# Optimization experiments

Hardware: AMD Instinct MI355X
Metric: run time of the kernel (lower is better)

Reference implementation:

```python
import jax, jax.numpy as jnp
import numpy as np

B, S, HID, NH = 4, 1024, 1024, 16
DK = HID // NH
SCALE = DK ** -0.5
NEG = -9e15


def setup_inputs() -> dict:
    key = jax.random.key(0)
    ks = jax.random.split(key, 10)
    std = HID ** -0.5
    return {
        "batch": jax.random.normal(ks[0], (B, S, HID), jnp.float32),
        "attn_bias": jax.random.normal(ks[1], (B, NH, S, S), jnp.float32),
        "Wq": jax.random.normal(ks[2], (HID, HID), jnp.float32) * std,
        "bq": jnp.zeros((HID,), jnp.float32),
        "Wk": jax.random.normal(ks[3], (HID, HID), jnp.float32) * std,
        "bk": jnp.zeros((HID,), jnp.float32),
        "Wv": jax.random.normal(ks[4], (HID, HID), jnp.float32) * std,
        "bv": jnp.zeros((HID,), jnp.float32),
        "Wo": jax.random.normal(ks[5], (HID, HID), jnp.float32) * std,
        "bo": jnp.zeros((HID,), jnp.float32),
    }


def reference(batch, attn_bias, Wq, bq, Wk, bk, Wv, bv, Wo, bo):
    b, s, _ = batch.shape
    # QKV projections -> [b, h, s, d]
    q = (batch @ Wq.T + bq).reshape(b, s, NH, DK).transpose(0, 2, 1, 3)
    k = (batch @ Wk.T + bk).reshape(b, s, NH, DK).transpose(0, 2, 1, 3)
    v = (batch @ Wv.T + bv).reshape(b, s, NH, DK).transpose(0, 2, 1, 3)
    # scaled scores [b, h, s, s]
    x = jnp.einsum("bhqd,bhkd->bhqk", q * SCALE, k)
    # custom zero-mask: exact zeros become -9e15
    x = jnp.where(x == 0, jnp.float32(NEG), x)
    x = x + attn_bias
    p = jax.nn.softmax(x, axis=3)  # dropout_rate=0.0 -> identity
    o = jnp.einsum("bhqk,bhkd->bhqd", p, v)
    o = o.transpose(0, 2, 1, 3).reshape(b, s, NH * DK)
    return o @ Wo.T + bo
```

## Files before the change

### kernel.cpp

```cpp
#include <hip/hip_runtime.h>
#include <hip/hip_bf16.h>
#include <stdint.h>
#include <stddef.h>

#define Bd  4
#define Sd  1024
#define Hd  1024
#define NHd 16
#define DKd 64
#define SCALEF 0.125f
#define NEGV  -9.0e15f
#define L2E   1.4426950408889634f

typedef __attribute__((ext_vector_type(8))) short bfrag;
typedef __attribute__((ext_vector_type(4))) float facc;
typedef __attribute__((ext_vector_type(4))) float f32x4;

typedef __attribute__((address_space(1))) const unsigned int ga_u32;
typedef __attribute__((address_space(3))) unsigned int ls_u32;

__device__ __forceinline__ void gload_lds16(const void* g, void* l) {
  __builtin_amdgcn_global_load_lds((ga_u32*)g, (ls_u32*)l, 16, 0, 0);
}

__device__ __forceinline__ unsigned short f2bf(float f) {
  unsigned int u = __float_as_uint(f);
  u += 0x7fffu + ((u >> 16) & 1u);
  return (unsigned short)(u >> 16);
}

__global__ void castk_all(const float* __restrict__ s0, const float* __restrict__ s1,
                          const float* __restrict__ s2, const float* __restrict__ s3,
                          const float* __restrict__ s4,
                          unsigned short* __restrict__ d0, unsigned short* __restrict__ d1,
                          unsigned short* __restrict__ d2, unsigned short* __restrict__ d3,
                          unsigned short* __restrict__ d4) {
  const int id = blockIdx.x;
  const float* s; unsigned short* d; int i;
  if (id < 4096) { s = s0; d = d0; i = id * 256 + threadIdx.x; }
  else {
    const int w = (id - 4096) >> 10;
    s = (w == 0) ? s1 : (w == 1) ? s2 : (w == 2) ? s3 : s4;
    d = (w == 0) ? d1 : (w == 1) ? d2 : (w == 2) ? d3 : d4;
    i = ((id - 4096) & 1023) * 256 + threadIdx.x;
  }
  float4 v = ((const float4*)s)[i];
  ushort4 ov;
  ov.x = f2bf(v.x); ov.y = f2bf(v.y); ov.z = f2bf(v.z); ov.w = f2bf(v.w);
  ((ushort4*)d)[i] = ov;
}

__global__ __launch_bounds__(256, 3)
void gemm_qkv(const unsigned short* __restrict__ A,
              const unsigned short* __restrict__ W0, const unsigned short* __restrict__ W1,
              const unsigned short* __restrict__ W2,
              const float* __restrict__ b0, const float* __restrict__ b1, const float* __restrict__ b2,
              unsigned short* __restrict__ o0, unsigned short* __restrict__ o1, unsigned short* __restrict__ o2) {
  __shared__ __align__(16) unsigned short smem[128 * 136];
  const int z = blockIdx.z;
  const unsigned short* Bm = (z == 0) ? W0 : (z == 1) ? W1 : W2;
  const float* bias = (z == 0) ? b0 : (z == 1) ? b1 : b2;
  unsigned short* out = (z == 0) ? o0 : (z == 1) ? o1 : o2;

  const int m0 = blockIdx.x * 128, n0 = blockIdx.y * 128;
  const int tid = threadIdx.x;
  const int wave = tid >> 6, lane = tid & 63;
  const int quad = lane >> 4, l16 = lane & 15;
  const int wm = wave >> 1, wn = wave & 1;

  facc acc[4][4] = {};

  const int j0 = wave * 128 + lane;
  const int j1 = j0 + 64;
  const int row0 = j0 >> 2, ko0 = (j0 & 3) << 3;
  const int row1 = j1 >> 2, ko1 = (j1 & 3) << 3;
  const size_t aoff0 = (size_t)(m0 + row0) * 1024 + ko0;
  const size_t aoff1 = (size_t)(m0 + row1) * 1024 + ko1;
  const size_t boff0 = (size_t)(n0 + row0) * 1024 + ko0;
  const size_t boff1 = (size_t)(n0 + row1) * 1024 + ko1;

  const int stA = (wave * 2 + 0) * 512;
  const int stA1i = (wave * 2 + 1) * 512;

  gload_lds16(A + aoff0, smem + stA);
  gload_lds16(A + aoff1, smem + stA1i);
  gload_lds16(Bm + boff0, smem + 8192 + stA);
  gload_lds16(Bm + boff1, smem + 8192 + stA1i);
  __syncthreads();

  for (int k0 = 0; k0 < 1024; k0 += 32) {
    const int cur = (k0 >> 5) & 1;
    const int nxt = cur ^ 1;
    if (k0 < 992) {
      unsigned short* dA = smem + nxt * 4096;
      unsigned short* dB = smem + 8192 + nxt * 4096;
      gload_lds16(A + aoff0 + k0 + 32, dA + stA);
      gload_lds16(A + aoff1 + k0 + 32, dA + stA1i);
      gload_lds16(Bm + boff0 + k0 + 32, dB + stA);
      gload_lds16(Bm + boff1 + k0 + 32, dB + stA1i);
    }
    const unsigned short* sA = smem + cur * 4096;
    const unsigned short* sB = smem + 8192 + cur * 4096;
    bfrag af[4], bf[4];
#pragma unroll
    for (int i = 0; i < 4; ++i) af[i] = *(const bfrag*)(sA + (wm * 64 + i * 16 + l16) * 32 + quad * 8);
#pragma unroll
    for (int j = 0; j < 4; ++j) bf[j] = *(const bfrag*)(sB + (wn * 64 + j * 16 + l16) * 32 + quad * 8);
#pragma unroll
    for (int i = 0; i < 4; ++i)
#pragma unroll
      for (int j = 0; j < 4; ++j)
        acc[i][j] = __builtin_amdgcn_mfma_f32_16x16x32_bf16(af[i], bf[j], acc[i][j], 0, 0, 0);
    __syncthreads();
  }

  if (z < 2) {
#pragma unroll
    for (int i = 0; i < 4; ++i)
#pragma unroll
      for (int j = 0; j < 4; ++j) {
        const int col = n0 + wn * 64 + j * 16 + l16;
        const float bv = bias[col];
        const int h = col >> 6, d = col & 63;
#pragma unroll
        for (int r = 0; r < 4; ++r) {
          const int m = m0 + wm * 64 + i * 16 + quad * 4 + r;
          const int b = m >> 10, s = m & 1023;
          out[(((size_t)(b * NHd + h) * Sd) + s) * DKd + d] = f2bf(acc[i][j][r] + bv);
        }
      }
  } else {
    unsigned short* sT = smem;
#pragma unroll
    for (int i = 0; i < 4; ++i)
#pragma unroll
      for (int j = 0; j < 4; ++j) {
        const int col = n0 + wn * 64 + j * 16 + l16;
        const float bv = bias[col];
        const int nrow = wn * 64 + j * 16 + l16;
        const int mbase = wm * 64 + i * 16 + quad * 4;
        ushort4 pk;
        pk.x = f2bf(acc[i][j][0] + bv);
        pk.y = f2bf(acc[i][j][1] + bv);
        pk.z = f2bf(acc[i][j][2] + bv);
        pk.w = f2bf(acc[i][j][3] + bv);
        *(ushort4*)(sT + nrow * 136 + mbase) = pk;
      }
    __syncthreads();
    const int bI = m0 >> 10, s0i = m0 & 1023;
#pragma unroll
    for (int it = 0; it < 8; ++it) {
      const int c = tid + it * 256;
      const int row = c >> 4, mc = (c & 15) * 8;
      bfrag vv = *(const bfrag*)(sT + row * 136 + mc);
      const int col = n0 + row, hh = col >> 6, dd = col & 63;
      *(bfrag*)(out + (((size_t)(bI * NHd + hh) * DKd) + dd) * Sd + s0i + mc) = vv;
    }
  }
}

__global__ __launch_bounds__(256, 3)
void gemm_out(const unsigned short* __restrict__ A, const unsigned short* __restrict__ Bm,
              const float* __restrict__ bias, float* __restrict__ out) {
  __shared__ __align__(16) unsigned short smem[24576];
  const int m0 = blockIdx.x * 64, n0 = blockIdx.y * 128;
  const int tid = threadIdx.x;
  const int wave = tid >> 6, lane = tid & 63;
  const int quad = lane >> 4, l16 = lane & 15;

  facc acc[8] = {};

  const int cA0 = (wave * 2 + 0) * 64 + lane;
  const int cA1 = (wave * 2 + 1) * 64 + lane;
  const int rA0 = cA0 >> 3, kA0 = ((cA0 & 7) ^ (rA0 & 7)) * 8;
  const int rA1 = cA1 >> 3, kA1 = ((cA1 & 7) ^ (rA1 & 7)) * 8;
  const size_t aoff0 = (size_t)(m0 + rA0) * 1024 + kA0;
  const size_t aoff1 = (size_t)(m0 + rA1) * 1024 + kA1;
  size_t boff[4];
#pragma unroll
  for (int i = 0; i < 4; ++i) {
    const int c = (wave * 4 + i) * 64 + lane;
    const int r = c >> 3, kk = ((c & 7) ^ (r & 7)) * 8;
    boff[i] = (size_t)(n0 + r) * 1024 + kk;
  }

  const int stA0 = (wave * 2 + 0) * 512;
  const int stA1i = (wave * 2 + 1) * 512;

  gload_lds16(A + aoff0, smem + stA0);
  gload_lds16(A + aoff1, smem + stA1i);
#pragma unroll
  for (int i = 0; i < 4; ++i)
    gload_lds16(Bm + boff[i], smem + 8192 + (wave * 4 + i) * 512);
  __syncthreads();

  for (int k0 = 0; k0 < 1024; k0 += 64) {
    const int cur = (k0 >> 6) & 1;
    const int nxt = cur ^ 1;
    if (k0 < 960) {
      unsigned short* dA = smem + nxt * 4096;
      unsigned short* dB = smem + 8192 + nxt * 8192;
      gload_lds16(A + aoff0 + k0 + 64, dA + stA0);
      gload_lds16(A + aoff1 + k0 + 64, dA + stA1i);
#pragma unroll
      for (int i = 0; i < 4; ++i)
        gload_lds16(Bm + boff[i] + k0 + 64, dB + (wave * 4 + i) * 512);
    }
    const unsigned short* sA = smem + cur * 4096;
    const unsigned short* sB = smem + 8192 + cur * 8192;
#pragma unroll
    for (int c2 = 0; c2 < 2; ++c2) {
      const int ko = ((c2 * 4 + quad) ^ (l16 & 7)) * 8;
      bfrag af = *(const bfrag*)(sA + (wave * 16 + l16) * 64 + ko);
#pragma unroll
      for (int j = 0; j < 8; ++j) {
        bfrag bf = *(const bfrag*)(sB + (j * 16 + l16) * 64 + ko);
        acc[j] = __builtin_amdgcn_mfma_f32_16x16x32_bf16(af, bf, acc[j], 0, 0, 0);
      }
    }
    __syncthreads();
  }

#pragma unroll
  for (int j = 0; j < 8; ++j) {
    const int col = n0 + j * 16 + l16;
    const float bv = bias[col];
#pragma unroll
    for (int r = 0; r < 4; ++r) {
      const int m = m0 + wave * 16 + quad * 4 + r;
      out[(size_t)m * 1024 + col] = acc[j][r] + bv;
    }
  }
}

__global__ __attribute__((amdgpu_flat_work_group_size(512, 512), amdgpu_waves_per_eu(4, 4)))
void attn_kernel(const unsigned short* __restrict__ q,
                 const unsigned short* __restrict__ k,
                 const unsigned short* __restrict__ vt,
                 const float* __restrict__ bias,
                 unsigned short* __restrict__ o)
{
  __shared__ __align__(16) unsigned short sK[2][64 * 64];
  __shared__ __align__(16) unsigned short sV[2][64 * 64];
  __shared__ __align__(16) unsigned int sP[8][16][36];

  const int p = blockIdx.x;
  const int xcd = p & 7;
  const int g = p >> 3;
  const int bh = ((g >> 3) << 3) | xcd;
  const int qblk = g & 7;
  const int tid = threadIdx.x;
  const int wave = tid >> 6, lane = tid & 63;
  const int quad = lane >> 4, l16 = lane & 15;
  const int b = bh >> 4, h = bh & 15;

  const unsigned short* qh = q + (size_t)bh * Sd * DKd;
  const unsigned short* kh = k + (size_t)bh * Sd * DKd;
  const unsigned short* vh = vt + (size_t)bh * DKd * Sd;
  const float* bias_h = bias + (size_t)bh * Sd * Sd;
  const int rq = qblk * 128 + wave * 16;
  unsigned int (*sPw)[36] = sP[wave];

  const int srow = wave * 8 + (lane >> 3);
  const int sslot = (lane & 7) ^ (srow & 7);
  const unsigned short* srcK = kh + (size_t)srow * DKd + sslot * 8;
  const unsigned short* srcV = vh + (size_t)srow * Sd + sslot * 8;
  unsigned short* dK0 = sK[0] + wave * 512;
  unsigned short* dK1 = sK[1] + wave * 512;
  unsigned short* dV0 = sV[0] + wave * 512;
  unsigned short* dV1 = sV[1] + wave * 512;

  const int xs0 = ((0 + quad) ^ (l16 & 7)) * 8;
  const int xs1 = ((4 + quad) ^ (l16 & 7)) * 8;

  bfrag qf[2];
#pragma unroll
  for (int c = 0; c < 2; ++c)
    qf[c] = *(const bfrag*)(qh + (size_t)(rq + l16) * DKd + c * 32 + quad * 8);

  facc oacc[4] = {};
  float lsum = 0.f;
  const float SL2 = SCALEF * L2E;

  const float* bpS = bias_h + (size_t)(rq + l16) * Sd + quad * 4;
  f32x4 br0 = __builtin_nontemporal_load((const f32x4*)(bpS + 0));
  f32x4 br1 = __builtin_nontemporal_load((const f32x4*)(bpS + 16));
  f32x4 br2 = __builtin_nontemporal_load((const f32x4*)(bpS + 32));
  f32x4 br3 = __builtin_nontemporal_load((const f32x4*)(bpS + 48));

  gload_lds16(srcK, dK0);
  gload_lds16(srcV, dV0);
  __syncthreads();

  for (int t = 0; t < 16; ++t) {
    const int bb = t & 1;
    if (t < 15) {
      const int kn = (t + 1) * 64;
      gload_lds16(srcK + (size_t)kn * DKd, bb ? dK0 : dK1);
      gload_lds16(srcV + kn, bb ? dV0 : dV1);
    }
    const unsigned short* sKb = sK[bb];
    const unsigned short* sVb = sV[bb];
    facc sacc[4] = {};
#pragma unroll
    for (int j = 0; j < 4; ++j) {
      bfrag kf = *(const bfrag*)(sKb + (j * 16 + l16) * 64 + xs0);
      sacc[j] = __builtin_amdgcn_mfma_f32_16x16x32_bf16(kf, qf[0], sacc[j], 0, 0, 0);
    }
#pragma unroll
    for (int j = 0; j < 4; ++j) {
      bfrag kf = *(const bfrag*)(sKb + (j * 16 + l16) * 64 + xs1);
      sacc[j] = __builtin_amdgcn_mfma_f32_16x16x32_bf16(kf, qf[1], sacc[j], 0, 0, 0);
    }
    asm volatile("" : "+v"(br0), "+v"(br1), "+v"(br2), "+v"(br3));
    unsigned int pk[4][2];
#pragma unroll
    for (int j = 0; j < 4; ++j) {
      const f32x4 bv = (j == 0) ? br0 : (j == 1) ? br1 : (j == 2) ? br2 : br3;
      float e0 = __builtin_amdgcn_exp2f(fmaf(sacc[j][0], SL2, bv.x * L2E));
      float e1 = __builtin_amdgcn_exp2f(fmaf(sacc[j][1], SL2, bv.y * L2E));
      float e2 = __builtin_amdgcn_exp2f(fmaf(sacc[j][2], SL2, bv.z * L2E));
      float e3 = __builtin_amdgcn_exp2f(fmaf(sacc[j][3], SL2, bv.w * L2E));
      e0 = (sacc[j][0] == 0.f) ? 0.f : e0;
      e1 = (sacc[j][1] == 0.f) ? 0.f : e1;
      e2 = (sacc[j][2] == 0.f) ? 0.f : e2;
      e3 = (sacc[j][3] == 0.f) ? 0.f : e3;
      lsum += (e0 + e1) + (e2 + e3);
      pk[j][0] = (unsigned int)f2bf(e0) | ((unsigned int)f2bf(e1) << 16);
      pk[j][1] = (unsigned int)f2bf(e2) | ((unsigned int)f2bf(e3) << 16);
    }
    if (t < 15) {
      const float* bpn = bpS + (t + 1) * 64;
      br0 = __builtin_nontemporal_load((const f32x4*)(bpn + 0));
      br1 = __builtin_nontemporal_load((const f32x4*)(bpn + 16));
      br2 = __builtin_nontemporal_load((const f32x4*)(bpn + 32));
      br3 = __builtin_nontemporal_load((const f32x4*)(bpn + 48));
    }
#pragma unroll
    for (int j = 0; j < 4; ++j) {
      uint2 w; w.x = pk[j][0]; w.y = pk[j][1];
      *(uint2*)&sPw[l16][j * 8 + quad * 2] = w;
    }
#pragma unroll
    for (int c = 0; c < 2; ++c) {
      bfrag pf = *(const bfrag*)&sPw[l16][c * 16 + quad * 4];
      const int xsc = c ? xs1 : xs0;
#pragma unroll
      for (int n = 0; n < 4; ++n) {
        bfrag vf = *(const bfrag*)(sVb + (n * 16 + l16) * 64 + xsc);
        oacc[n] = __builtin_amdgcn_mfma_f32_16x16x32_bf16(vf, pf, oacc[n], 0, 0, 0);
      }
    }
    __syncthreads();
  }

  lsum += __shfl_xor(lsum, 16, 64);
  lsum += __shfl_xor(lsum, 32, 64);
  const float rinv = 1.0f / lsum;

  const size_t rowo = (size_t)(b * Sd + rq + l16) * Hd + h * 64 + quad * 4;
#pragma unroll
  for (int n = 0; n < 4; ++n) {
    ushort4 st;
    st.x = f2bf(oacc[n][0] * rinv);
    st.y = f2bf(oacc[n][1] * rinv);
    st.z = f2bf(oacc[n][2] * rinv);
    st.w = f2bf(oacc[n][3] * rinv);
    *(ushort4*)(o + rowo + n * 16) = st;
  }
}

extern "C" void kernel_launch(void* const* d_in, const int* in_sizes, int n_in,
                              void* d_out, int out_size, void* d_ws, size_t ws_size,
                              hipStream_t stream) {
  const float* batch = (const float*)d_in[0];
  const float* attn_bias = (const float*)d_in[1];
  const float* Wq = (const float*)d_in[2];
  const float* bq = (const float*)d_in[3];
  const float* Wk = (const float*)d_in[4];
  const float* bk = (const float*)d_in[5];
  const float* Wv = (const float*)d_in[6];
  const float* bv = (const float*)d_in[7];
  const float* Wo = (const float*)d_in[8];
  const float* bo = (const float*)d_in[9];
  float* out = (float*)d_out;

  unsigned short* ws = (unsigned short*)d_ws;
  unsigned short* Ab  = ws;
  unsigned short* Wqb = Ab  + 4194304;
  unsigned short* Wkb = Wqb + 1048576;
  unsigned short* Wvb = Wkb + 1048576;
  unsigned short* Wob = Wvb + 1048576;
  unsigned short* qb  = Wob + 1048576;
  unsigned short* kb  = qb  + 4194304;
  unsigned short* vtb = kb  + 4194304;
  unsigned short* ob  = vtb + 4194304;

  castk_all<<<8192, 256, 0, stream>>>(batch, Wq, Wk, Wv, Wo, Ab, Wqb, Wkb, Wvb, Wob);
  gemm_qkv<<<dim3(32, 8, 3), 256, 0, stream>>>(Ab, Wqb, Wkb, Wvb, bq, bk, bv, qb, kb, vtb);
  attn_kernel<<<dim3(512), 512, 0, stream>>>(qb, kb, vtb, attn_bias, ob);
  gemm_out<<<dim3(64, 8), 256, 0, stream>>>(ob, Wob, bo, out);
}
```

Before: 450.2 us.

## Stage attention bias through LDS via async loads and halve KV tile size

The attention kernel now streams the fp32 bias tile for the whole 128-row query block into double-buffered LDS using global_load_lds, instead of each wave holding per-row bias registers loaded with nontemporal loads. The key/value tile shrinks from 64 to 32 keys per iteration (32 iterations), with all 512 threads cooperating on K/V staging and new swizzles for the narrower V tile. The waves_per_eu hint is removed. This aims to get coalesced asynchronous bias loads and lower register pressure, at the cost of more iterations and barriers and more LDS use.

Result: slower. 478.3 us (+6.2%).

```diff
diff --git a/kernel.cpp b/kernel.cpp
--- a/kernel.cpp
+++ b/kernel.cpp
@@ -233,16 +233,17 @@
   }
 }
 
-__global__ __attribute__((amdgpu_flat_work_group_size(512, 512), amdgpu_waves_per_eu(4, 4)))
+__global__ __attribute__((amdgpu_flat_work_group_size(512, 512)))
 void attn_kernel(const unsigned short* __restrict__ q,
                  const unsigned short* __restrict__ k,
                  const unsigned short* __restrict__ vt,
                  const float* __restrict__ bias,
                  unsigned short* __restrict__ o)
 {
-  __shared__ __align__(16) unsigned short sK[2][64 * 64];
-  __shared__ __align__(16) unsigned short sV[2][64 * 64];
-  __shared__ __align__(16) unsigned int sP[8][16][36];
+  __shared__ __align__(16) unsigned short sK[2][2048];
+  __shared__ __align__(16) unsigned short sV[2][2048];
+  __shared__ __align__(16) float sB[2][4096];
+  __shared__ __align__(16) unsigned int sP[8][16][20];
 
   const int p = blockIdx.x;
   const int xcd = p & 7;
@@ -258,20 +259,25 @@
   const unsigned short* kh = k + (size_t)bh * Sd * DKd;
   const unsigned short* vh = vt + (size_t)bh * DKd * Sd;
   const float* bias_h = bias + (size_t)bh * Sd * Sd;
-  const int rq = qblk * 128 + wave * 16;
-  unsigned int (*sPw)[36] = sP[wave];
-
-  const int srow = wave * 8 + (lane >> 3);
-  const int sslot = (lane & 7) ^ (srow & 7);
-  const unsigned short* srcK = kh + (size_t)srow * DKd + sslot * 8;
-  const unsigned short* srcV = vh + (size_t)srow * Sd + sslot * 8;
-  unsigned short* dK0 = sK[0] + wave * 512;
-  unsigned short* dK1 = sK[1] + wave * 512;
-  unsigned short* dV0 = sV[0] + wave * 512;
-  unsigned short* dV1 = sV[1] + wave * 512;
-
-  const int xs0 = ((0 + quad) ^ (l16 & 7)) * 8;
-  const int xs1 = ((4 + quad) ^ (l16 & 7)) * 8;
+  const int q0 = qblk * 128;
+  const int rq = q0 + wave * 16;
+  unsigned int (*sPw)[20] = sP[wave];
+
+  const int cKV = tid & 255;
+  const int isV = tid >> 8;
+  const int krow = cKV >> 3, kslot = (cKV & 7) ^ (krow & 7);
+  const int vrow = cKV >> 2, vslot = (cKV & 3) ^ ((vrow ^ (vrow >> 2)) & 3);
+  const unsigned short* srcKV = isV ? (vh + (size_t)vrow * Sd + vslot * 8)
+                                    : (kh + (size_t)krow * DKd + kslot * 8);
+  const int kvTileStep = isV ? 32 : 32 * DKd;
+  const int dKVoff = (wave & 3) * 512;
+  const int bc0 = tid, bc1 = tid + 512;
+  const int brow0 = bc0 >> 3, bslot0 = (bc0 & 7) ^ (brow0 & 7);
+  const int brow1 = bc1 >> 3, bslot1 = (bc1 & 7) ^ (brow1 & 7);
+  const float* srcB0 = bias_h + (size_t)(q0 + brow0) * Sd + bslot0 * 4;
+  const float* srcB1 = bias_h + (size_t)(q0 + brow1) * Sd + bslot1 * 4;
+  const int dB0 = wave * 256;
+  const int dB1 = 2048 + wave * 256;
 
   bfrag qf[2];
 #pragma unroll
@@ -282,41 +288,35 @@
   float lsum = 0.f;
   const float SL2 = SCALEF * L2E;
 
-  const float* bpS = bias_h + (size_t)(rq + l16) * Sd + quad * 4;
-  f32x4 br0 = __builtin_nontemporal_load((const f32x4*)(bpS + 0));
-  f32x4 br1 = __builtin_nontemporal_load((const f32x4*)(bpS + 16));
-  f32x4 br2 = __builtin_nontemporal_load((const f32x4*)(bpS + 32));
-  f32x4 br3 = __builtin_nontemporal_load((const f32x4*)(bpS + 48));
-
-  gload_lds16(srcK, dK0);
-  gload_lds16(srcV, dV0);
+  gload_lds16(srcKV, (isV ? sV[0] : sK[0]) + dKVoff);
+  gload_lds16(srcB0, sB[0] + dB0);
+  gload_lds16(srcB1, sB[0] + dB1);
   __syncthreads();
 
-  for (int t = 0; t < 16; ++t) {
+  for (int t = 0; t < 32; ++t) {
     const int bb = t & 1;
-    if (t < 15) {
-      const int kn = (t + 1) * 64;
-      gload_lds16(srcK + (size_t)kn * DKd, bb ? dK0 : dK1);
-      gload_lds16(srcV + kn, bb ? dV0 : dV1);
-    }
-    const unsigned short* sKb = sK[bb];
-    const unsigned short* sVb = sV[bb];
-    facc sacc[4] = {};
-#pragma unroll
-    for (int j = 0; j < 4; ++j) {
-      bfrag kf = *(const bfrag*)(sKb + (j * 16 + l16) * 64 + xs0);
-      sacc[j] = __builtin_amdgcn_mfma_f32_16x16x32_bf16(kf, qf[0], sacc[j], 0, 0, 0);
-    }
-#pragma unroll
-    for (int j = 0; j < 4; ++j) {
-      bfrag kf = *(const bfrag*)(sKb + (j * 16 + l16) * 64 + xs1);
-      sacc[j] = __builtin_amdgcn_mfma_f32_16x16x32_bf16(kf, qf[1], sacc[j], 0, 0, 0);
-    }
-    asm volatile("" : "+v"(br0), "+v"(br1), "+v"(br2), "+v"(br3));
-    unsigned int pk[4][2];
-#pragma unroll
-    for (int j = 0; j < 4; ++j) {
-      const f32x4 bv = (j == 0) ? br0 : (j == 1) ? br1 : (j == 2) ? br2 : br3;
+    if (t < 31) {
+      const int adv = (t + 1) * kvTileStep;
+      gload_lds16(srcKV + adv, (isV ? sV[bb ^ 1] : sK[bb ^ 1]) + dKVoff);
+      gload_lds16(srcB0 + (t + 1) * 32, sB[bb ^ 1] + dB0);
+      gload_lds16(srcB1 + (t + 1) * 32, sB[bb ^ 1] + dB1);
+    }
+    facc sacc[2] = {};
+#pragma unroll
+    for (int cc = 0; cc < 2; ++cc)
+#pragma unroll
+      for (int j = 0; j < 2; ++j) {
+        const int row = j * 16 + l16;
+        const int slot = ((cc * 4 + quad) ^ (row & 7));
+        bfrag kf = *(const bfrag*)(sK[bb] + row * 64 + slot * 8);
+        sacc[j] = __builtin_amdgcn_mfma_f32_16x16x32_bf16(kf, qf[cc], sacc[j], 0, 0, 0);
+      }
+    unsigned int pk[2][2];
+#pragma unroll
+    for (int j = 0; j < 2; ++j) {
+      const int brow = wave * 16 + l16;
+      const int bslot = (j * 4 + quad) ^ (brow & 7);
+      const f32x4 bv = *(const f32x4*)(sB[bb] + brow * 32 + bslot * 4);
       float e0 = __builtin_amdgcn_exp2f(fmaf(sacc[j][0], SL2, bv.x * L2E));
       float e1 = __builtin_amdgcn_exp2f(fmaf(sacc[j][1], SL2, bv.y * L2E));
       float e2 = __builtin_amdgcn_exp2f(fmaf(sacc[j][2], SL2, bv.z * L2E));
@@ -329,25 +329,18 @@
       pk[j][0] = (unsigned int)f2bf(e0) | ((unsigned int)f2bf(e1) << 16);
       pk[j][1] = (unsigned int)f2bf(e2) | ((unsigned int)f2bf(e3) << 16);
     }
-    if (t < 15) {
-      const float* bpn = bpS + (t + 1) * 64;
-      br0 = __builtin_nontemporal_load((const f32x4*)(bpn + 0));
-      br1 = __builtin_nontemporal_load((const f32x4*)(bpn + 16));
-      br2 = __builtin_nontemporal_load((const f32x4*)(bpn + 32));
-      br3 = __builtin_nontemporal_load((const f32x4*)(bpn + 48));
-    }
-#pragma unroll
-    for (int j = 0; j < 4; ++j) {
+#pragma unroll
+    for (int j = 0; j < 2; ++j) {
       uint2 w; w.x = pk[j][0]; w.y = pk[j][1];
       *(uint2*)&sPw[l16][j * 8 + quad * 2] = w;
     }
-#pragma unroll
-    for (int c = 0; c < 2; ++c) {
-      bfrag pf = *(const bfrag*)&sPw[l16][c * 16 + quad * 4];
-      const int xsc = c ? xs1 : xs0;
+    {
+      bfrag pf = *(const bfrag*)&sPw[l16][quad * 4];
 #pragma unroll
       for (int n = 0; n < 4; ++n) {
-        bfrag vf = *(const bfrag*)(sVb + (n * 16 + l16) * 64 + xsc);
+        const int row = n * 16 + l16;
+        const int slot = quad ^ ((row ^ (row >> 2)) & 3);
+        bfrag vf = *(const bfrag*)(sV[bb] + row * 32 + slot * 8);
         oacc[n] = __builtin_amdgcn_mfma_f32_16x16x32_bf16(vf, pf, oacc[n], 0, 0, 0);
       }
     }
```
